# Optimization experiments

Measured on AMD Instinct MI355X. Metric: run time of the kernel, lower is better.

Reference implementation:

```python
import jax, jax.numpy as jnp
import numpy as np
import math

B, T, D, H = 2, 2048, 2048, 16
HD = D // H  # head_dim = 128


def setup_inputs() -> dict:
    key = jax.random.key(0)
    ks = jax.random.split(key, 9)
    s = 1.0 / math.sqrt(D)
    return {
        "x": jax.random.normal(ks[0], (B, T, D), dtype=jnp.float32),
        "Wq": jax.random.normal(ks[1], (D, D), dtype=jnp.float32) * s,
        "bq": jax.random.normal(ks[2], (D,), dtype=jnp.float32) * 0.01,
        "Wk": jax.random.normal(ks[3], (D, D), dtype=jnp.float32) * s,
        "bk": jax.random.normal(ks[4], (D,), dtype=jnp.float32) * 0.01,
        "Wv": jax.random.normal(ks[5], (D, D), dtype=jnp.float32) * s,
        "bv": jax.random.normal(ks[6], (D,), dtype=jnp.float32) * 0.01,
        "Wo": jax.random.normal(ks[7], (D, D), dtype=jnp.float32) * s,
        "bo": jax.random.normal(ks[8], (D,), dtype=jnp.float32) * 0.01,
    }


def reference(x, Wq, bq, Wk, bk, Wv, bv, Wo, bo):
    b, t, c = x.shape
    # projections; split heads: (B,T,D) -> (B,H,T,HD)
    def split_heads(y):
        return y.reshape(b, t, H, HD).transpose(0, 2, 1, 3)

    q = split_heads(x @ Wq + bq)
    k = split_heads(x @ Wk + bk)
    v = split_heads(x @ Wv + bv)

    scale = 1.0 / math.sqrt(HD)
    attn = jnp.einsum('bhqd,bhkd->bhqk', q, k) * scale  # (B,H,T,T)
    # causal mask (prefill path: past_k is None)
    causal = jnp.tril(jnp.ones((t, t), dtype=bool))
    attn = jnp.where(causal, attn, -jnp.inf)
    attn = jax.nn.softmax(attn, axis=-1)
    out = jnp.einsum('bhqk,bhkd->bhqd', attn, v)  # (B,H,T,HD)
    out = out.transpose(0, 2, 1, 3).reshape(b, t, c)
    out = out @ Wo + bo
    return (out, k, v)
```

## Files before the change

### kernel.cpp

```cpp
#include <hip/hip_runtime.h>
#include <hip/hip_bf16.h>

#define B_ 2
#define T_ 2048
#define D_ 2048
#define H_ 16
#define HD_ 128
#define M_ 4096

typedef __attribute__((ext_vector_type(8))) short short8;
typedef __attribute__((ext_vector_type(8))) __bf16 bf16x8;
typedef __attribute__((ext_vector_type(4))) float f32x4;
typedef __attribute__((ext_vector_type(4))) unsigned uint32x4;

__device__ __forceinline__ short f2bf(float f) {
  unsigned u = __builtin_bit_cast(unsigned, f);
  u += 0x7fffu + ((u >> 16) & 1u);
  return (short)(u >> 16);
}

__device__ __forceinline__ unsigned cvtpk(float lo, float hi) {
  unsigned r;
  asm("v_cvt_pk_bf16_f32 %0, %1, %2" : "=v"(r) : "v"(lo), "v"(hi));
  return r;
}

__device__ __forceinline__ void gl_lds16(const void* g, void* l) {
  __builtin_amdgcn_global_load_lds(
      (const __attribute__((address_space(1))) unsigned int*)g,
      (__attribute__((address_space(3))) unsigned int*)l, 16, 0, 0);
}

__device__ __forceinline__ f32x4 mfma_bf16(short8 a, short8 b, f32x4 c) {
  return __builtin_amdgcn_mfma_f32_16x16x32_bf16(
      __builtin_bit_cast(bf16x8, a), __builtin_bit_cast(bf16x8, b), c, 0, 0, 0);
}

__device__ __forceinline__ float2 sw16f(float x) {
  float a = x, bv;
  asm("v_mov_b32 %0, %1" : "=v"(bv) : "v"(x));
  asm("v_permlane16_swap_b32 %0, %1" : "+v"(a), "+v"(bv));
  return make_float2(a, bv);
}
__device__ __forceinline__ float2 sw32f(float x) {
  float a = x, bv;
  asm("v_mov_b32 %0, %1" : "=v"(bv) : "v"(x));
  asm("v_permlane32_swap_b32 %0, %1" : "+v"(a), "+v"(bv));
  return make_float2(a, bv);
}
__device__ __forceinline__ void sw16u(unsigned x, unsigned& e, unsigned& o) {
  unsigned a = x, bv;
  asm("v_mov_b32 %0, %1" : "=v"(bv) : "v"(x));
  asm("v_permlane16_swap_b32 %0, %1" : "+v"(a), "+v"(bv));
  e = a; o = bv;
}
__device__ __forceinline__ void pl32u(unsigned& a, unsigned& b) {
  asm("v_permlane32_swap_b32 %0, %1" : "+v"(a), "+v"(b));
}

__global__ void cast_f32_bf16(const float* __restrict__ in, short* __restrict__ out, int n4) {
  int i = blockIdx.x * blockDim.x + threadIdx.x;
  int stride = gridDim.x * blockDim.x;
  for (; i < n4; i += stride) {
    float4 v = ((const float4*)in)[i];
    short4 s;
    s.x = f2bf(v.x); s.y = f2bf(v.y); s.z = f2bf(v.z); s.w = f2bf(v.w);
    ((short4*)out)[i] = s;
  }
}

__global__ void transpose_cast_w4(const float* __restrict__ Wq, const float* __restrict__ Wk,
                                  const float* __restrict__ Wv, const float* __restrict__ Wo,
                                  short* __restrict__ wqkv, short* __restrict__ wo) {
  __shared__ float t[32][33];
  int z = blockIdx.z;
  const float* W = z == 0 ? Wq : z == 1 ? Wk : z == 2 ? Wv : Wo;
  short* dst = z < 3 ? wqkv + (size_t)z * D_ * D_ : wo;
  int n0 = blockIdx.x * 32, k0 = blockIdx.y * 32;
  int tx = threadIdx.x, ty = threadIdx.y;
#pragma unroll
  for (int j = 0; j < 4; ++j)
    t[ty + j * 8][tx] = W[(size_t)(k0 + ty + j * 8) * D_ + n0 + tx];
  __syncthreads();
#pragma unroll
  for (int j = 0; j < 4; ++j)
    dst[(size_t)(n0 + ty + j * 8) * D_ + k0 + tx] = f2bf(t[tx][ty + j * 8]);
}

__global__ __launch_bounds__(512, 2) void gemm_qkv(
    const short* __restrict__ A, const short* __restrict__ Bt,
    const float* __restrict__ b0, const float* __restrict__ b1,
    const float* __restrict__ b2,
    short* __restrict__ q_o, short* __restrict__ k_o,
    float* __restrict__ kf_o, float* __restrict__ vf_o,
    short* __restrict__ vt_o) {
  __shared__ __attribute__((aligned(16))) char lds[2][57344];
  const int K = D_, NT = K / 64;

  int d = blockIdx.x;
  int lg = (d & 7) * 64 + (d >> 3);
  int m0 = (lg & 15) * 256, n0 = (lg >> 4) * 192;

  int tid = threadIdx.x, lane = tid & 63, wid = tid >> 6;
  int wm = wid >> 2, wn = wid & 3;
  int lr = lane & 15, g = lane >> 4;

  int rowA = tid >> 2;
  int cA = ((((tid & 3) << 4) ^ (((rowA >> 1) & 3) << 4)) >> 1);
  const short* aS = A + (size_t)(m0 + rowA) * K + cA;
  int rowB = tid >> 3;
  int cB = ((((tid & 7) << 4) ^ ((rowB & 7) << 4)) >> 1);
  const short* bS = Bt + (size_t)(n0 + rowB) * K + cB;
  char* ldsb = (char*)lds;

  auto stageA = [&](int ts, int kh) {
    char* dst = ldsb + (ts & 1) * 57344 + kh * 16384 + tid * 16;
    const short* s = aS + ts * 64 + kh * 32;
    gl_lds16(s, dst);
    gl_lds16(s + (size_t)128 * K, dst + 8192);
  };
  auto stageB = [&](int ts) {
    char* dst = ldsb + (ts & 1) * 57344 + 32768 + tid * 16;
    const short* s = bS + ts * 64;
    gl_lds16(s, dst);
    gl_lds16(s + (size_t)64 * K, dst + 8192);
    gl_lds16(s + (size_t)128 * K, dst + 16384);
  };

  int swzA = (g * 16) ^ (((lr >> 1) & 3) << 4);
  int aoff = (wm * 128 + lr) * 64 + swzA;
  int boff0 = (wn * 48 + lr) * 128 + ((g * 16) ^ ((lr & 7) << 4));
  int boff1 = (wn * 48 + lr) * 128 + ((64 + g * 16) ^ ((lr & 7) << 4));

  f32x4 acc[8][3] = {};

  stageA(0, 0); stageA(0, 1); stageB(0); stageA(1, 0);
  asm volatile("s_waitcnt vmcnt(2)" ::: "memory");
  __builtin_amdgcn_s_barrier();
  __builtin_amdgcn_sched_barrier(0);

#pragma unroll 1
  for (int t = 0; t < NT; ++t) {
    const char* base = ldsb + (t & 1) * 57344;
    int t1 = (t + 1 < NT) ? t + 1 : NT - 1;
    int t2 = (t + 2 < NT) ? t + 2 : NT - 1;
    short8 afr[4], bfr[3];

#pragma unroll
    for (int mi = 0; mi < 4; ++mi) afr[mi] = *(const short8*)(base + aoff + mi * 1024);
#pragma unroll
    for (int ni = 0; ni < 3; ++ni) bfr[ni] = *(const short8*)(base + 32768 + boff0 + ni * 2048);
    stageA(t1, 1);
    __builtin_amdgcn_s_barrier();
    asm volatile("s_waitcnt lgkmcnt(0)" ::: "memory");
    __builtin_amdgcn_sched_barrier(0);
    __builtin_amdgcn_s_setprio(1);
#pragma unroll
    for (int mi = 0; mi < 4; ++mi)
#pragma unroll
      for (int ni = 0; ni < 3; ++ni)
        acc[mi][ni] = mfma_bf16(afr[mi], bfr[ni], acc[mi][ni]);
    __builtin_amdgcn_s_setprio(0);
    __builtin_amdgcn_s_barrier();
    __builtin_amdgcn_sched_barrier(0);

#pragma unroll
    for (int mi = 0; mi < 4; ++mi) afr[mi] = *(const short8*)(base + aoff + (4 + mi) * 1024);
    stageB(t1);
    __builtin_amdgcn_s_barrier();
    asm volatile("s_waitcnt lgkmcnt(0)" ::: "memory");
    __builtin_amdgcn_sched_barrier(0);
    __builtin_amdgcn_s_setprio(1);
#pragma unroll
    for (int mi = 0; mi < 4; ++mi)
#pragma unroll
      for (int ni = 0; ni < 3; ++ni)
        acc[4 + mi][ni] = mfma_bf16(afr[mi], bfr[ni], acc[4 + mi][ni]);
    __builtin_amdgcn_s_setprio(0);
    __builtin_amdgcn_s_barrier();
    __builtin_amdgcn_sched_barrier(0);

#pragma unroll
    for (int mi = 0; mi < 4; ++mi) afr[mi] = *(const short8*)(base + 16384 + aoff + mi * 1024);
#pragma unroll
    for (int ni = 0; ni < 3; ++ni) bfr[ni] = *(const short8*)(base + 32768 + boff1 + ni * 2048);
    stageA(t2, 0);
    __builtin_amdgcn_s_barrier();
    asm volatile("s_waitcnt lgkmcnt(0)" ::: "memory");
    __builtin_amdgcn_sched_barrier(0);
    __builtin_amdgcn_s_setprio(1);
#pragma unroll
    for (int mi = 0; mi < 4; ++mi)
#pragma unroll
      for (int ni = 0; ni < 3; ++ni)
        acc[mi][ni] = mfma_bf16(afr[mi], bfr[ni], acc[mi][ni]);
    __builtin_amdgcn_s_setprio(0);
    __builtin_amdgcn_s_barrier();
    __builtin_amdgcn_sched_barrier(0);

#pragma unroll
    for (int mi = 0; mi < 4; ++mi) afr[mi] = *(const short8*)(base + 16384 + aoff + (4 + mi) * 1024);
    __builtin_amdgcn_s_barrier();
    asm volatile("s_waitcnt lgkmcnt(0)" ::: "memory");
    __builtin_amdgcn_sched_barrier(0);
    __builtin_amdgcn_s_setprio(1);
#pragma unroll
    for (int mi = 0; mi < 4; ++mi)
#pragma unroll
      for (int ni = 0; ni < 3; ++ni)
        acc[4 + mi][ni] = mfma_bf16(afr[mi], bfr[ni], acc[4 + mi][ni]);
    __builtin_amdgcn_s_setprio(0);
    asm volatile("s_waitcnt vmcnt(2)" ::: "memory");
    __builtin_amdgcn_s_barrier();
    __builtin_amdgcn_sched_barrier(0);
  }

#pragma unroll
  for (int ni = 0; ni < 3; ++ni) {
    int gcb = n0 + wn * 48 + ni * 16;
    int region = gcb >> 11;
    int nc = (gcb & 2047) + lr;
    int hh = nc >> 7, hd = nc & 127;
    const float* bias = region == 0 ? b0 : region == 1 ? b1 : b2;
    float bv = bias[nc];
#pragma unroll
    for (int mi = 0; mi < 8; ++mi) {
      int gr0 = m0 + wm * 128 + mi * 16 + (g << 2);
      int bb = gr0 >> 11, tt0 = gr0 & 2047;
      size_t hbase = (size_t)(bb * H_ + hh);
      float v0 = acc[mi][ni][0] + bv;
      float v1 = acc[mi][ni][1] + bv;
      float v2 = acc[mi][ni][2] + bv;
      float v3 = acc[mi][ni][3] + bv;
      size_t ib = (hbase * T_ + tt0) * HD_ + hd;
      if (region == 0) {
        q_o[ib] = f2bf(v0); q_o[ib + HD_] = f2bf(v1);
        q_o[ib + 2 * HD_] = f2bf(v2); q_o[ib + 3 * HD_] = f2bf(v3);
      } else if (region == 1) {
        k_o[ib] = f2bf(v0); k_o[ib + HD_] = f2bf(v1);
        k_o[ib + 2 * HD_] = f2bf(v2); k_o[ib + 3 * HD_] = f2bf(v3);
        kf_o[ib] = v0; kf_o[ib + HD_] = v1;
        kf_o[ib + 2 * HD_] = v2; kf_o[ib + 3 * HD_] = v3;
      } else {
        vf_o[ib] = v0; vf_o[ib + HD_] = v1;
        vf_o[ib + 2 * HD_] = v2; vf_o[ib + 3 * HD_] = v3;
        short4 s4;
        s4.x = f2bf(v0); s4.y = f2bf(v1); s4.z = f2bf(v2); s4.w = f2bf(v3);
        *(short4*)&vt_o[(hbase * HD_ + hd) * T_ + tt0] = s4;
      }
    }
  }
}

__global__ __launch_bounds__(256, 2) void gemm_rb(
    const short* __restrict__ A, const short* __restrict__ Bt,
    const float* __restrict__ b0, float* __restrict__ f_o) {
  __shared__ __attribute__((aligned(16))) short lds[4][2][4096];
  const int K = D_, NT = K / 32;

  int nx = gridDim.x, nwg = nx * gridDim.y;
  int d = blockIdx.y * nx + blockIdx.x;
  int cpx = nwg >> 3;
  int lg = (d & 7) * cpx + (d >> 3);
  int m0 = (lg / nx) * 128, n0 = (lg % nx) * 128;

  int tid = threadIdx.x, lane = tid & 63, w = tid >> 6;
  int wm = w >> 1, wn = w & 1;
  int lr = lane & 15, g = lane >> 4;

  int o1 = tid * 16, o2 = 4096 + tid * 16;
  int row1 = tid >> 2, row2 = 64 + row1;
  int cb = (tid & 3) << 4;
  int c1 = (cb ^ (((row1 >> 1) & 3) << 4)) >> 1;
  int c2 = (cb ^ (((row2 >> 1) & 3) << 4)) >> 1;
  const short* aS1 = A + (size_t)(m0 + row1) * K + c1;
  const short* aS2 = A + (size_t)(m0 + row2) * K + c2;
  const short* bS1 = Bt + (size_t)(n0 + row1) * K + c1;
  const short* bS2 = Bt + (size_t)(n0 + row2) * K + c2;

  int aoff[4], boff[4];
#pragma unroll
  for (int i = 0; i < 4; ++i) {
    int ra = wm * 64 + i * 16 + lr;
    aoff[i] = ra * 64 + ((g * 16) ^ (((ra >> 1) & 3) << 4));
    int rb = wn * 64 + i * 16 + lr;
    boff[i] = rb * 64 + ((g * 16) ^ (((rb >> 1) & 3) << 4));
  }

  f32x4 acc[4][4] = {};

#pragma unroll
  for (int s = 0; s < 3; ++s) {
    char* la = (char*)&lds[s][0][0];
    char* lb = (char*)&lds[s][1][0];
    gl_lds16(aS1 + s * 32, la + o1);
    gl_lds16(aS2 + s * 32, la + o2);
    gl_lds16(bS1 + s * 32, lb + o1);
    gl_lds16(bS2 + s * 32, lb + o2);
  }
  asm volatile("s_waitcnt vmcnt(8)" ::: "memory");
  __builtin_amdgcn_s_barrier();
  __builtin_amdgcn_sched_barrier(0);

#pragma unroll 1
  for (int t4 = 0; t4 < NT; t4 += 4) {
#pragma unroll
    for (int p = 0; p < 4; ++p) {
      int t = t4 + p;
      {
        int ts = (t + 3 < NT) ? t + 3 : NT - 1;
        char* la = (char*)&lds[(p + 3) & 3][0][0];
        char* lb = (char*)&lds[(p + 3) & 3][1][0];
        gl_lds16(aS1 + ts * 32, la + o1);
        gl_lds16(aS2 + ts * 32, la + o2);
        gl_lds16(bS1 + ts * 32, lb + o1);
        gl_lds16(bS2 + ts * 32, lb + o2);
      }
      const char* la = (const char*)&lds[p][0][0];
      const char* lb = (const char*)&lds[p][1][0];
      short8 af[4], bfv[4];
#pragma unroll
      for (int i = 0; i < 4; ++i) {
        af[i] = *(const short8*)(la + aoff[i]);
        bfv[i] = *(const short8*)(lb + boff[i]);
      }
      __builtin_amdgcn_s_setprio(1);
#pragma unroll
      for (int mi = 0; mi < 4; ++mi)
#pragma unroll
        for (int ni = 0; ni < 4; ++ni)
          acc[mi][ni] = mfma_bf16(af[mi], bfv[ni], acc[mi][ni]);
      __builtin_amdgcn_s_setprio(0);
      asm volatile("s_waitcnt vmcnt(8)" ::: "memory");
      __builtin_amdgcn_s_barrier();
      __builtin_amdgcn_sched_barrier(0);
    }
  }

#pragma unroll
  for (int mi = 0; mi < 4; ++mi) {
#pragma unroll
    for (int ni = 0; ni < 4; ++ni) {
      int gr0 = m0 + wm * 64 + mi * 16 + (g << 2);
      int gc = n0 + wn * 64 + ni * 16 + lr;
      float bv = b0[gc];
#pragma unroll
      for (int r = 0; r < 4; ++r)
        f_o[(size_t)(gr0 + r) * D_ + gc] = acc[mi][ni][r] + bv;
    }
  }
}

__global__ __launch_bounds__(256, 2) void attn_fwd(
    const short* __restrict__ qb, const short* __restrict__ kb,
    const short* __restrict__ vtb, short* __restrict__ aob) {
  __shared__ __attribute__((aligned(16))) char kvlds[2][16384];

  int d = blockIdx.y * gridDim.x + blockIdx.x;
  int lg = (d & 7) * 64 + (d >> 3);
  int bh = lg >> 4, jx = lg & 15;

  int tid = threadIdx.x, w = tid >> 6, lane = tid & 63;
  int lr = lane & 15, g = lane >> 4;
  const short* Q  = qb  + (size_t)bh * T_ * HD_;
  const short* Kp = kb  + (size_t)bh * T_ * HD_;
  const short* Vt = vtb + (size_t)bh * HD_ * T_;
  const float scale = 0.08838834764831845f;
  int b = bh >> 4, h = bh & 15;
  bool hi16 = (lane & 16) != 0;

  int oA = ((2 * w + 0) * 64 + lane) * 16;
  int oB = ((2 * w + 1) * 64 + lane) * 16;
  int rKA = oA >> 8, rKB = oB >> 8;
  size_t skA = (size_t)rKA * HD_ + (((oA & 255) ^ ((rKA & 7) << 4)) >> 1);
  size_t skB = (size_t)rKB * HD_ + (((oB & 255) ^ ((rKB & 7) << 4)) >> 1);
  int rVA = oA >> 6, rVB = oB >> 6;
  size_t svA = (size_t)rVA * T_ + (((oA & 63) ^ (((rVA >> 1) & 3) << 4)) >> 1);
  size_t svB = (size_t)rVB * T_ + (((oB & 63) ^ (((rVB >> 1) & 3) << 4)) >> 1);

#pragma unroll 1
  for (int pass = 0; pass < 2; ++pass) {
    int qt = pass ? (31 - jx) : jx;
    int q0 = qt * 64 + w * 16;
    int ntiles = 2 * qt + 2;

    {
      char* kd = &kvlds[0][0];
      char* vd = &kvlds[0][8192];
      gl_lds16(Kp + skA, kd + oA);
      gl_lds16(Kp + skB, kd + oB);
      gl_lds16(Vt + svA, vd + oA);
      gl_lds16(Vt + svB, vd + oB);
    }

    short8 qf[4];
#pragma unroll
    for (int kk = 0; kk < 4; ++kk)
      qf[kk] = *(const short8*)&Q[(size_t)(q0 + lr) * HD_ + kk * 32 + g * 8];

    f32x4 o[8] = {};
    float mrow = -1e30f, lrow = 0.f;
    __syncthreads();

#pragma unroll 1
    for (int t = 0; t < ntiles; ++t) {
      int kv0 = t * 32, buf = t & 1;
      if (t + 1 < ntiles) {
        char* kd = &kvlds[buf ^ 1][0];
        char* vd = &kvlds[buf ^ 1][8192];
        const short* Kn = Kp + (size_t)(kv0 + 32) * HD_;
        const short* Vn = Vt + (kv0 + 32);
        gl_lds16(Kn + skA, kd + oA);
        gl_lds16(Kn + skB, kd + oB);
        gl_lds16(Vn + svA, vd + oA);
        gl_lds16(Vn + svB, vd + oB);
      }
      if (kv0 < q0 + 16) {
        const char* kb_ = &kvlds[buf][0];
        const char* vb_ = &kvlds[buf][8192];
        short8 kf0[4], kf1[4], vf[8];
#pragma unroll
        for (int kk = 0; kk < 4; ++kk) {
          int cs = (kk * 64 + g * 16) ^ ((lr & 7) << 4);
          kf0[kk] = *(const short8*)(kb_ + (lr * 256 + cs));
          kf1[kk] = *(const short8*)(kb_ + ((16 + lr) * 256 + cs));
        }
#pragma unroll
        for (int f = 0; f < 8; ++f)
          vf[f] = *(const short8*)(vb_ + ((f * 16 + lr) * 64 +
                   ((g * 16) ^ (((lr >> 1) & 3) << 4))));

        f32x4 s0 = {}, s1 = {};
        __builtin_amdgcn_s_setprio(1);
#pragma unroll
        for (int kk = 0; kk < 4; ++kk) {
          s0 = mfma_bf16(kf0[kk], qf[kk], s0);
          s1 = mfma_bf16(kf1[kk], qf[kk], s1);
        }
        __builtin_amdgcn_s_setprio(0);

        float vv[8];
#pragma unroll
        for (int r = 0; r < 4; ++r) {
          vv[r] = s0[r] * scale;
          vv[4 + r] = s1[r] * scale;
        }
        if (kv0 + 31 > q0) {
          int qrow = q0 + lr;
#pragma unroll
          for (int r = 0; r < 4; ++r) {
            if (kv0 + 4 * g + r > qrow) vv[r] = -1e30f;
            if (kv0 + 16 + 4 * g + r > qrow) vv[4 + r] = -1e30f;
          }
        }

        float pm = vv[0];
#pragma unroll
        for (int i = 1; i < 8; ++i) pm = fmaxf(pm, vv[i]);
        { float2 tpm = sw32f(pm); pm = fmaxf(tpm.x, tpm.y); }
        { float2 tpm = sw16f(pm); pm = fmaxf(tpm.x, tpm.y); }

        bool rescale = !__all(pm - mrow <= 8.0f);
        float alpha = 1.0f;
        if (rescale) {
          float mnew = fmaxf(mrow, pm);
          alpha = __expf(mrow - mnew);
          mrow = mnew;
        }

        float p[8];
        float rs = 0.f;
#pragma unroll
        for (int i = 0; i < 8; ++i) { p[i] = __expf(vv[i] - mrow); rs += p[i]; }
        { float2 trs = sw32f(rs); rs = trs.x + trs.y; }
        { float2 trs = sw16f(rs); rs = trs.x + trs.y; }
        lrow = (rescale ? lrow * alpha : lrow) + rs;

        if (rescale) {
          float alr[4];
#pragma unroll
          for (int r = 0; r < 4; ++r) alr[r] = __shfl(alpha, 4 * g + r);
#pragma unroll
          for (int f = 0; f < 8; ++f)
#pragma unroll
            for (int r = 0; r < 4; ++r) o[f][r] *= alr[r];
        }

        unsigned w0 = cvtpk(p[0], p[1]), w1 = cvtpk(p[2], p[3]);
        unsigned w2 = cvtpk(p[4], p[5]), w3 = cvtpk(p[6], p[7]);
        unsigned e0, od0, e1, od1, e2, od2, e3, od3;
        sw16u(w0, e0, od0); sw16u(w1, e1, od1);
        sw16u(w2, e2, od2); sw16u(w3, e3, od3);
        unsigned F0 = e0,  S0 = e2;  pl32u(F0, S0);
        unsigned F1 = e1,  S1 = e3;  pl32u(F1, S1);
        unsigned F2 = od0, S2 = od2; pl32u(F2, S2);
        unsigned F3 = od1, S3 = od3; pl32u(F3, S3);
        uint32x4 paw = { hi16 ? S0 : F0, hi16 ? S1 : F1,
                         hi16 ? S2 : F2, hi16 ? S3 : F3 };
        short8 pa = __builtin_bit_cast(short8, paw);

        __builtin_amdgcn_s_setprio(1);
#pragma unroll
        for (int f = 0; f < 8; ++f) o[f] = mfma_bf16(pa, vf[f], o[f]);
        __builtin_amdgcn_s_setprio(0);
      }
      __syncthreads();
    }

    float inv = 1.0f / lrow;
    float invr[4];
#pragma unroll
    for (int r = 0; r < 4; ++r) invr[r] = __shfl(inv, 4 * g + r);
#pragma unroll
    for (int r = 0; r < 4; ++r) {
      int q = q0 + 4 * g + r;
      size_t rowoff = ((size_t)(b * T_ + q)) * D_ + h * HD_;
#pragma unroll
      for (int f = 0; f < 8; ++f)
        aob[rowoff + f * 16 + lr] = f2bf(o[f][r] * invr[r]);
    }
  }
}

extern "C" void kernel_launch(void* const* d_in, const int* in_sizes, int n_in,
                              void* d_out, int out_size, void* d_ws, size_t ws_size,
                              hipStream_t stream) {
  const float* x  = (const float*)d_in[0];
  const float* Wq = (const float*)d_in[1];
  const float* bq = (const float*)d_in[2];
  const float* Wk = (const float*)d_in[3];
  const float* bk = (const float*)d_in[4];
  const float* Wv = (const float*)d_in[5];
  const float* bv = (const float*)d_in[6];
  const float* Wo = (const float*)d_in[7];
  const float* bo = (const float*)d_in[8];
  float* out  = (float*)d_out;
  float* kout = out + (size_t)M_ * D_;
  float* vout = kout + (size_t)M_ * D_;

  char* ws = (char*)d_ws;
  auto alloc = [&](size_t bytes) {
    char* p = ws;
    ws += (bytes + 255) & ~(size_t)255;
    return p;
  };
  short* xb    = (short*)alloc((size_t)M_ * D_ * 2);
  short* wqkvT = (short*)alloc((size_t)3 * D_ * D_ * 2);
  short* woT   = (short*)alloc((size_t)D_ * D_ * 2);
  short* qb    = (short*)alloc((size_t)M_ * D_ * 2);
  short* kb    = (short*)alloc((size_t)M_ * D_ * 2);
  short* vtb   = (short*)alloc((size_t)M_ * D_ * 2);
  short* aob = xb;

  cast_f32_bf16<<<2048, 256, 0, stream>>>(x, xb, M_ * D_ / 4);
  dim3 tb(32, 8);
  transpose_cast_w4<<<dim3(64, 64, 4), tb, 0, stream>>>(Wq, Wk, Wv, Wo, wqkvT, woT);

  gemm_qkv<<<512, 512, 0, stream>>>(xb, wqkvT, bq, bk, bv, qb, kb, kout, vout, vtb);
  attn_fwd<<<dim3(16, 32), 256, 0, stream>>>(qb, kb, vtb, aob);
  gemm_rb<<<dim3(16, 32), 256, 0, stream>>>(aob, woT, bo, out);
}
```

Before: 255.1 us.

## Widen QKV GEMM tile to 256x256 with unified staging of A and B

Changes the fused QKV projection GEMM from 256x192 tiles (512 blocks) to 256x256 tiles (384 blocks). A and B are now staged through a single lambda with matching swizzle, and LDS grows to 128 KB double-buffered. Each wave computes 8x4 MFMA tiles instead of 8x3 and loads all B fragments for both k-halves up front. The goal is higher arithmetic intensity and fewer global loads per FLOP. The cost is more registers and LDS per block, which limits occupancy to one block per CU, and a grid of 384 blocks that may fill the 256 CUs unevenly.

```diff
diff --git a/kernel.cpp b/kernel.cpp
--- a/kernel.cpp
+++ b/kernel.cpp
@@ -94,63 +94,56 @@
     short* __restrict__ q_o, short* __restrict__ k_o,
     float* __restrict__ kf_o, float* __restrict__ vf_o,
     short* __restrict__ vt_o) {
-  __shared__ __attribute__((aligned(16))) char lds[2][57344];
+  __shared__ __attribute__((aligned(16))) char lds[131072];
   const int K = D_, NT = K / 64;
 
   int d = blockIdx.x;
-  int lg = (d & 7) * 64 + (d >> 3);
-  int m0 = (lg & 15) * 256, n0 = (lg >> 4) * 192;
+  int lg = (d & 7) * 48 + (d >> 3);
+  int m0 = (lg & 15) * 256, n0 = (lg >> 4) * 256;
 
   int tid = threadIdx.x, lane = tid & 63, wid = tid >> 6;
   int wm = wid >> 2, wn = wid & 3;
   int lr = lane & 15, g = lane >> 4;
 
-  int rowA = tid >> 2;
-  int cA = ((((tid & 3) << 4) ^ (((rowA >> 1) & 3) << 4)) >> 1);
-  const short* aS = A + (size_t)(m0 + rowA) * K + cA;
-  int rowB = tid >> 3;
-  int cB = ((((tid & 7) << 4) ^ ((rowB & 7) << 4)) >> 1);
-  const short* bS = Bt + (size_t)(n0 + rowB) * K + cB;
+  int scol = ((((tid & 3) << 4) ^ (((tid >> 3) & 3) << 4)) >> 1);
+  const short* aS = A + (size_t)(m0 + (tid >> 2)) * K + scol;
+  const short* bS = Bt + (size_t)(n0 + (tid >> 2)) * K + scol;
   char* ldsb = (char*)lds;
 
-  auto stageA = [&](int ts, int kh) {
-    char* dst = ldsb + (ts & 1) * 57344 + kh * 16384 + tid * 16;
-    const short* s = aS + ts * 64 + kh * 32;
+  auto stage = [&](int ts, int hid) {
+    char* dst = ldsb + (ts & 1) * 65536 + hid * 16384 + tid * 16;
+    const short* s = ((hid & 2) ? bS : aS) + ts * 64 + (hid & 1) * 32;
     gl_lds16(s, dst);
     gl_lds16(s + (size_t)128 * K, dst + 8192);
   };
-  auto stageB = [&](int ts) {
-    char* dst = ldsb + (ts & 1) * 57344 + 32768 + tid * 16;
-    const short* s = bS + ts * 64;
-    gl_lds16(s, dst);
-    gl_lds16(s + (size_t)64 * K, dst + 8192);
-    gl_lds16(s + (size_t)128 * K, dst + 16384);
-  };
-
-  int swzA = (g * 16) ^ (((lr >> 1) & 3) << 4);
-  int aoff = (wm * 128 + lr) * 64 + swzA;
-  int boff0 = (wn * 48 + lr) * 128 + ((g * 16) ^ ((lr & 7) << 4));
-  int boff1 = (wn * 48 + lr) * 128 + ((64 + g * 16) ^ ((lr & 7) << 4));
-
-  f32x4 acc[8][3] = {};
-
-  stageA(0, 0); stageA(0, 1); stageB(0); stageA(1, 0);
-  asm volatile("s_waitcnt vmcnt(2)" ::: "memory");
+
+  int fsw = (g * 16) ^ (((lr >> 1) & 3) << 4);
+  int aoff = (wm * 128 + lr) * 64 + fsw;
+  int boff = 32768 + (wn * 64 + lr) * 64 + fsw;
+
+  f32x4 acc[8][4] = {};
+
+  stage(0, 0); stage(0, 2); stage(0, 1); stage(0, 3);
+  stage(1, 0); stage(1, 2);
+  asm volatile("s_waitcnt vmcnt(4)" ::: "memory");
   __builtin_amdgcn_s_barrier();
   __builtin_amdgcn_sched_barrier(0);
 
 #pragma unroll 1
   for (int t = 0; t < NT; ++t) {
-    const char* base = ldsb + (t & 1) * 57344;
+    const char* base = ldsb + (t & 1) * 65536;
     int t1 = (t + 1 < NT) ? t + 1 : NT - 1;
     int t2 = (t + 2 < NT) ? t + 2 : NT - 1;
-    short8 afr[4], bfr[3];
-
+    short8 afr[4], bfr[4][2];
+
+#pragma unroll
+    for (int ni = 0; ni < 4; ++ni) {
+      bfr[ni][0] = *(const short8*)(base + boff + ni * 1024);
+      bfr[ni][1] = *(const short8*)(base + 16384 + boff + ni * 1024);
+    }
 #pragma unroll
     for (int mi = 0; mi < 4; ++mi) afr[mi] = *(const short8*)(base + aoff + mi * 1024);
-#pragma unroll
-    for (int ni = 0; ni < 3; ++ni) bfr[ni] = *(const short8*)(base + 32768 + boff0 + ni * 2048);
-    stageA(t1, 1);
+    stage(t1, 1);
     __builtin_amdgcn_s_barrier();
     asm volatile("s_waitcnt lgkmcnt(0)" ::: "memory");
     __builtin_amdgcn_sched_barrier(0);
@@ -158,15 +151,15 @@
 #pragma unroll
     for (int mi = 0; mi < 4; ++mi)
 #pragma unroll
-      for (int ni = 0; ni < 3; ++ni)
-        acc[mi][ni] = mfma_bf16(afr[mi], bfr[ni], acc[mi][ni]);
+      for (int ni = 0; ni < 4; ++ni)
+        acc[mi][ni] = mfma_bf16(afr[mi], bfr[ni][0], acc[mi][ni]);
     __builtin_amdgcn_s_setprio(0);
     __builtin_amdgcn_s_barrier();
     __builtin_amdgcn_sched_barrier(0);
 
 #pragma unroll
     for (int mi = 0; mi < 4; ++mi) afr[mi] = *(const short8*)(base + aoff + (4 + mi) * 1024);
-    stageB(t1);
+    stage(t1, 3);
     __builtin_amdgcn_s_barrier();
     asm volatile("s_waitcnt lgkmcnt(0)" ::: "memory");
     __builtin_amdgcn_sched_barrier(0);
@@ -174,17 +167,16 @@
 #pragma unroll
     for (int mi = 0; mi < 4; ++mi)
 #pragma unroll
-      for (int ni = 0; ni < 3; ++ni)
-        acc[4 + mi][ni] = mfma_bf16(afr[mi], bfr[ni], acc[4 + mi][ni]);
+      for (int ni = 0; ni < 4; ++ni)
+        acc[4 + mi][ni] = mfma_bf16(afr[mi], bfr[ni][0], acc[4 + mi][ni]);
     __builtin_amdgcn_s_setprio(0);
+    asm volatile("s_waitcnt vmcnt(4)" ::: "memory");
     __builtin_amdgcn_s_barrier();
     __builtin_amdgcn_sched_barrier(0);
 
 #pragma unroll
     for (int mi = 0; mi < 4; ++mi) afr[mi] = *(const short8*)(base + 16384 + aoff + mi * 1024);
-#pragma unroll
-    for (int ni = 0; ni < 3; ++ni) bfr[ni] = *(const short8*)(base + 32768 + boff1 + ni * 2048);
-    stageA(t2, 0);
+    stage(t2, 0);
     __builtin_amdgcn_s_barrier();
     asm volatile("s_waitcnt lgkmcnt(0)" ::: "memory");
     __builtin_amdgcn_sched_barrier(0);
@@ -192,14 +184,15 @@
 #pragma unroll
     for (int mi = 0; mi < 4; ++mi)
 #pragma unroll
-      for (int ni = 0; ni < 3; ++ni)
-        acc[mi][ni] = mfma_bf16(afr[mi], bfr[ni], acc[mi][ni]);
+      for (int ni = 0; ni < 4; ++ni)
+        acc[mi][ni] = mfma_bf16(afr[mi], bfr[ni][1], acc[mi][ni]);
     __builtin_amdgcn_s_setprio(0);
     __builtin_amdgcn_s_barrier();
     __builtin_amdgcn_sched_barrier(0);
 
 #pragma unroll
     for (int mi = 0; mi < 4; ++mi) afr[mi] = *(const short8*)(base + 16384 + aoff + (4 + mi) * 1024);
+    stage(t2, 2);
     __builtin_amdgcn_s_barrier();
     asm volatile("s_waitcnt lgkmcnt(0)" ::: "memory");
     __builtin_amdgcn_sched_barrier(0);
@@ -207,22 +200,21 @@
 #pragma unroll
     for (int mi = 0; mi < 4; ++mi)
 #pragma unroll
-      for (int ni = 0; ni < 3; ++ni)
-        acc[4 + mi][ni] = mfma_bf16(afr[mi], bfr[ni], acc[4 + mi][ni]);
+      for (int ni = 0; ni < 4; ++ni)
+        acc[4 + mi][ni] = mfma_bf16(afr[mi], bfr[ni][1], acc[4 + mi][ni]);
     __builtin_amdgcn_s_setprio(0);
-    asm volatile("s_waitcnt vmcnt(2)" ::: "memory");
-    __builtin_amdgcn_s_barrier();
-    __builtin_amdgcn_sched_barrier(0);
-  }
-
-#pragma unroll
-  for (int ni = 0; ni < 3; ++ni) {
-    int gcb = n0 + wn * 48 + ni * 16;
-    int region = gcb >> 11;
-    int nc = (gcb & 2047) + lr;
-    int hh = nc >> 7, hd = nc & 127;
-    const float* bias = region == 0 ? b0 : region == 1 ? b1 : b2;
-    float bv = bias[nc];
+    asm volatile("s_waitcnt vmcnt(4)" ::: "memory");
+    __builtin_amdgcn_s_barrier();
+    __builtin_amdgcn_sched_barrier(0);
+  }
+
+  int region = n0 >> 11, nc = n0 & 2047;
+  const float* bias = region == 0 ? b0 : region == 1 ? b1 : b2;
+#pragma unroll
+  for (int ni = 0; ni < 4; ++ni) {
+    int gc = nc + wn * 64 + ni * 16 + lr;
+    int hh = gc >> 7, hd = gc & 127;
+    float bv = bias[gc];
 #pragma unroll
     for (int mi = 0; mi < 8; ++mi) {
       int gr0 = m0 + wm * 128 + mi * 16 + (g << 2);
@@ -556,7 +548,7 @@
   dim3 tb(32, 8);
   transpose_cast_w4<<<dim3(64, 64, 4), tb, 0, stream>>>(Wq, Wk, Wv, Wo, wqkvT, woT);
 
-  gemm_qkv<<<512, 512, 0, stream>>>(xb, wqkvT, bq, bk, bv, qb, kb, kout, vout, vtb);
+  gemm_qkv<<<384, 512, 0, stream>>>(xb, wqkvT, bq, bk, bv, qb, kb, kout, vout, vtb);
   attn_fwd<<<dim3(16, 32), 256, 0, stream>>>(qb, kb, vtb, aob);
   gemm_rb<<<dim3(16, 32), 256, 0, stream>>>(aob, woT, bo, out);
 }
```

Measured after the change: 273.4 us. 7.2% more time.
